# Kernel tuning notes

Measured on AMD Instinct MI355X. Metric: run time of the kernel, lower is better.

## Reference

```python
import jax, jax.numpy as jnp
import numpy as np

FRAMES, RANK = 128, 5          # rank=5 implied by create_adj6 non_adj index lists (max index 4)
N = FRAMES * RANK              # 640 nodes
B, NFEAT, NHID, NCLASS = 128, 256, 8, 16
ALPHA = 0.2                    # LeakyReLU negative slope
MASK_VAL = -9e15               # hard mask value from the torch code


def create_adj6(frames, rank):
    """Block-diagonal (with holes) + chain adjacency, exactly as in the torch source."""
    adj = np.zeros((frames * rank, frames * rank), dtype=np.float32)
    non_adj_x = [0, 0, 1, 2, 3, 3, 4, 4]
    non_adj_y = [3, 4, 4, 3, 0, 2, 0, 1]
    for i in range(frames):
        adj[rank * i:rank * (i + 1), rank * i:rank * (i + 1)] = 1
        for j in range(len(non_adj_x)):
            adj[rank * i + non_adj_x[j], rank * i + non_adj_y[j]] = 0
        for j in range(rank):
            if i > 0:
                adj[rank * i + j, rank * (i - 1) + j] = 1
            if i < frames - 1:
                adj[rank * i + j, rank * (i + 1) + j] = 1
    return adj


def _xavier(key, shape):
    fan_in, fan_out = shape[0], shape[1]
    std = np.sqrt(2.0) * np.sqrt(2.0 / (fan_in + fan_out))  # gain=sqrt(2) xavier_normal
    return std * jax.random.normal(key, shape, dtype=jnp.float32)


def setup_inputs() -> dict:
    key = jax.random.key(0)
    ks = jax.random.split(key, 7)
    x = jax.random.normal(ks[0], (B, N, NFEAT), dtype=jnp.float32)
    W1 = _xavier(ks[1], (NFEAT, NHID))
    a11 = _xavier(ks[2], (NHID, 1))
    a12 = _xavier(ks[3], (NHID, 1))
    W2 = _xavier(ks[4], (NHID, NCLASS))  # nhid*nheads=8 -> nclass=16
    a21 = _xavier(ks[5], (NCLASS, 1))
    a22 = _xavier(ks[6], (NCLASS, 1))
    adj = jnp.asarray(create_adj6(FRAMES, RANK) > 0)  # bool [N, N]
    return dict(x=x, W1=W1, a11=a11, a12=a12, W2=W2, a21=a21, a22=a22, adj=adj)


def gat_layer(xi, adj, W, a1, a2):
    # xi: [N, F_in]
    h = xi @ W                              # [N, F_out]
    f1 = h @ a1                             # [N, 1]
    f2 = h @ a2                             # [N, 1]
    e = jax.nn.leaky_relu(f1 + f2.T, negative_slope=ALPHA)  # [N, N]
    scores = jnp.where(adj, e, jnp.float32(MASK_VAL))        # hard additive-style mask
    att = jax.nn.softmax(scores, axis=-1)   # dropout disabled (eval mode)
    return att @ h                          # [N, F_out]


def reference(x, W1, a11, a12, W2, a21, a22, adj):
    def single(xi):
        h1 = gat_layer(xi, adj, W1, a11, a12)          # concat=False -> no elu inside layer
        h2 = jax.nn.elu(gat_layer(h1, adj, W2, a21, a22))
        return jax.nn.log_softmax(h2, axis=1)          # [N, NCLASS]
    return jax.vmap(single)(x)                          # [B, N, NCLASS]
```

## Files before the change

kernel.cpp:

```cpp
#include <hip/hip_runtime.h>
#include <hip/hip_bf16.h>

#define B_ 128
#define N_ 640
#define NFEAT 256
#define NHID 8
#define NCLASS 16
#define RANK 5
#define FRAMES 128
#define ALPHA 0.2f
#define PACKMASK 30236135u

#define QSPLIT 4
#define TFRAMES (FRAMES / QSPLIT)
#define TCOUNT (TFRAMES * RANK)
#define BLOCKT 384
#define MAXSTAGE 180
#define H1S 9
#define H2S 17
#define W1TS 260
#define ROWSPP (BLOCKT / 4)

__device__ __forceinline__ float lrelu(float v) { return v >= 0.0f ? v : ALPHA * v; }

__global__ void __launch_bounds__(BLOCKT, 3) k_fused(
    const float* __restrict__ x, const float* __restrict__ W1,
    const float* __restrict__ a11, const float* __restrict__ a12,
    const float* __restrict__ W2, const float* __restrict__ a21, const float* __restrict__ a22,
    float* __restrict__ out)
{
    __shared__ float smem[MAXSTAGE * H2S + 2 * MAXSTAGE + NHID * W1TS];
    float* h1s = smem;
    float* f1s = smem + MAXSTAGE * H1S;
    float* f2s = f1s + MAXSTAGE;
    float* h2s = smem;
    float* g1s = smem + MAXSTAGE * H2S;
    float* g2s = g1s + MAXSTAGE;
    float* w1t = smem + MAXSTAGE * H2S + 2 * MAXSTAGE;

    const int bid = blockIdx.x;
    const int bq  = (bid & 7) * 64 + (bid >> 3);
    const int b   = bq >> 2;
    const int q   = bq & 3;

    const int tf_lo  = q * TFRAMES;
    const int l1f_lo = max(tf_lo - 1, 0);
    const int l1f_hi = min(tf_lo + TFRAMES, FRAMES - 1);
    const int stf_lo = max(tf_lo - 2, 0);
    const int stf_hi = min(tf_lo + TFRAMES + 1, FRAMES - 1);
    const int stage_lo  = stf_lo * RANK;
    const int stage_cnt = (stf_hi - stf_lo + 1) * RANK;
    const int l1_lo  = l1f_lo * RANK;
    const int l1_cnt = (l1f_hi - l1f_lo + 1) * RANK;
    const int t_lo   = tf_lo * RANK;

    const int tid = threadIdx.x;

    for (int idx = tid; idx < NFEAT * NHID; idx += BLOCKT) {
        const int f = idx >> 3, k = idx & 7;
        w1t[k * W1TS + f] = W1[idx];
    }
    __syncthreads();

    const int sub = tid & 3;
    const int rg  = tid >> 2;
#pragma unroll
    for (int p = 0; p < 2; ++p) {
        const int row = p * ROWSPP + rg;
        if (row < stage_cnt) {
            const float* xr = x + ((size_t)b * N_ + stage_lo + row) * NFEAT;
            float4 xv[16];
#pragma unroll
            for (int t = 0; t < 16; ++t)
                xv[t] = *reinterpret_cast<const float4*>(xr + t * 16 + sub * 4);

            float h[NHID];
#pragma unroll
            for (int k = 0; k < NHID; ++k) h[k] = 0.0f;
#pragma unroll
            for (int t = 0; t < 16; ++t) {
#pragma unroll
                for (int k = 0; k < NHID; ++k) {
                    const float4 wk = *reinterpret_cast<const float4*>(
                        &w1t[k * W1TS + t * 16 + sub * 4]);
                    h[k] = fmaf(xv[t].x, wk.x, h[k]);
                    h[k] = fmaf(xv[t].y, wk.y, h[k]);
                    h[k] = fmaf(xv[t].z, wk.z, h[k]);
                    h[k] = fmaf(xv[t].w, wk.w, h[k]);
                }
            }
#pragma unroll
            for (int k = 0; k < NHID; ++k) {
                h[k] += __shfl_xor(h[k], 1, 64);
                h[k] += __shfl_xor(h[k], 2, 64);
            }
            if (sub == 0) {
                float s1 = 0.0f, s2 = 0.0f;
#pragma unroll
                for (int k = 0; k < NHID; ++k) {
                    s1 = fmaf(h[k], a11[k], s1);
                    s2 = fmaf(h[k], a12[k], s2);
                    h1s[row * H1S + k] = h[k];
                }
                f1s[row] = s1;
                f2s[row] = s2;
            }
        }
    }
    __syncthreads();

    float h2[NCLASS];
    float s1g = 0.0f, s2g = 0.0f;
    const bool actL1 = (tid < l1_cnt);
    if (actL1) {
        const int u  = l1_lo + tid;
        const int fr = u / RANK;
        const int ru = u - fr * RANK;
        const unsigned rm = (PACKMASK >> (5 * ru)) & 31u;
        const int loc      = u - stage_lo;
        const int base_loc = fr * RANK - stage_lo;
        const bool hp = (fr > 0), hn = (fr < FRAMES - 1);
        const float fu = f1s[loc];

        float m = -1e30f;
        if (hp) m = fmaxf(m, lrelu(fu + f2s[loc - RANK]));
#pragma unroll
        for (int rv = 0; rv < RANK; ++rv)
            if (rm & (1u << rv)) m = fmaxf(m, lrelu(fu + f2s[base_loc + rv]));
        if (hn) m = fmaxf(m, lrelu(fu + f2s[loc + RANK]));

        float s = 0.0f;
        float o1[NHID];
#pragma unroll
        for (int k = 0; k < NHID; ++k) o1[k] = 0.0f;

        auto acc1 = [&](int vloc) {
            float w = __expf(lrelu(fu + f2s[vloc]) - m);
            s += w;
#pragma unroll
            for (int k = 0; k < NHID; ++k) o1[k] = fmaf(w, h1s[vloc * H1S + k], o1[k]);
        };
        if (hp) acc1(loc - RANK);
#pragma unroll
        for (int rv = 0; rv < RANK; ++rv)
            if (rm & (1u << rv)) acc1(base_loc + rv);
        if (hn) acc1(loc + RANK);

        const float inv = 1.0f / s;
#pragma unroll
        for (int k = 0; k < NHID; ++k) o1[k] *= inv;

#pragma unroll
        for (int c = 0; c < NCLASS; ++c) {
            float t = 0.0f;
#pragma unroll
            for (int k = 0; k < NHID; ++k) t = fmaf(o1[k], W2[k * NCLASS + c], t);
            h2[c] = t;
            s1g = fmaf(t, a21[c], s1g);
            s2g = fmaf(t, a22[c], s2g);
        }
    }
    __syncthreads();

    if (actL1) {
        const int loc = l1_lo + tid - stage_lo;
#pragma unroll
        for (int c = 0; c < NCLASS; ++c) h2s[loc * H2S + c] = h2[c];
        g1s[loc] = s1g;
        g2s[loc] = s2g;
    }
    __syncthreads();

    if (tid < TCOUNT) {
        const int u  = t_lo + tid;
        const int fr = u / RANK;
        const int ru = u - fr * RANK;
        const unsigned rm = (PACKMASK >> (5 * ru)) & 31u;
        const int loc      = u - stage_lo;
        const int base_loc = fr * RANK - stage_lo;
        const bool hp = (fr > 0), hn = (fr < FRAMES - 1);
        const float gu = g1s[loc];

        float m = -1e30f;
        if (hp) m = fmaxf(m, lrelu(gu + g2s[loc - RANK]));
#pragma unroll
        for (int rv = 0; rv < RANK; ++rv)
            if (rm & (1u << rv)) m = fmaxf(m, lrelu(gu + g2s[base_loc + rv]));
        if (hn) m = fmaxf(m, lrelu(gu + g2s[loc + RANK]));

        float s = 0.0f;
        float o2[NCLASS];
#pragma unroll
        for (int c = 0; c < NCLASS; ++c) o2[c] = 0.0f;

        auto acc2 = [&](int vloc) {
            float w = __expf(lrelu(gu + g2s[vloc]) - m);
            s += w;
#pragma unroll
            for (int c = 0; c < NCLASS; ++c) o2[c] = fmaf(w, h2s[vloc * H2S + c], o2[c]);
        };
        if (hp) acc2(loc - RANK);
#pragma unroll
        for (int rv = 0; rv < RANK; ++rv)
            if (rm & (1u << rv)) acc2(base_loc + rv);
        if (hn) acc2(loc + RANK);

        const float inv = 1.0f / s;
#pragma unroll
        for (int c = 0; c < NCLASS; ++c) o2[c] *= inv;

#pragma unroll
        for (int c = 0; c < NCLASS; ++c) o2[c] = (o2[c] > 0.0f) ? o2[c] : __expf(o2[c]) - 1.0f;

        float mm = o2[0];
#pragma unroll
        for (int c = 1; c < NCLASS; ++c) mm = fmaxf(mm, o2[c]);
        float ss = 0.0f;
#pragma unroll
        for (int c = 0; c < NCLASS; ++c) ss += __expf(o2[c] - mm);
        const float ls = mm + __logf(ss);

        float* op = out + ((size_t)b * N_ + u) * NCLASS;
#pragma unroll
        for (int c = 0; c < NCLASS; c += 4)
            *reinterpret_cast<float4*>(op + c) =
                make_float4(o2[c] - ls, o2[c + 1] - ls, o2[c + 2] - ls, o2[c + 3] - ls);
    }
}

extern "C" void kernel_launch(void* const* d_in, const int* in_sizes, int n_in,
                              void* d_out, int out_size, void* d_ws, size_t ws_size,
                              hipStream_t stream)
{
    const float* x   = (const float*)d_in[0];
    const float* W1  = (const float*)d_in[1];
    const float* a11 = (const float*)d_in[2];
    const float* a12 = (const float*)d_in[3];
    const float* W2  = (const float*)d_in[4];
    const float* a21 = (const float*)d_in[5];
    const float* a22 = (const float*)d_in[6];
    float* outp = (float*)d_out;

    k_fused<<<B_ * QSPLIT, BLOCKT, 0, stream>>>(x, W1, a11, a12, W2, a21, a22, outp);
}
```

Before: 26.93 us.

## Split batches into eight frame chunks and compute first projection per-thread with scalar W1 loads

Doubles the sequence split to eight chunks per batch with 256-thread blocks, so there are more, smaller blocks. The first-layer projection now gives each thread one full row half of 128 features and reads W1 directly from global memory with wave-uniform (scalar) addresses. This replaces the shared-memory transposed W1 copy and the cross-lane shuffle reduction. The two halves are combined through a shared partial buffer. The smaller chunks mean more halo rows are recomputed overall, and each thread holds 16 float4 loads, which raises register pressure.

```diff
diff --git a/kernel.cpp b/kernel.cpp
--- a/kernel.cpp
+++ b/kernel.cpp
@@ -1,5 +1,4 @@
 #include <hip/hip_runtime.h>
-#include <hip/hip_bf16.h>
 
 #define B_ 128
 #define N_ 640
@@ -11,37 +10,41 @@
 #define ALPHA 0.2f
 #define PACKMASK 30236135u
 
-#define QSPLIT 4
+#define QSPLIT 8
 #define TFRAMES (FRAMES / QSPLIT)
 #define TCOUNT (TFRAMES * RANK)
-#define BLOCKT 384
-#define MAXSTAGE 180
+#define BLOCKT 256
+#define MAXSTAGE 100
 #define H1S 9
 #define H2S 17
-#define W1TS 260
-#define ROWSPP (BLOCKT / 4)
+
+#define OFF_F1S (MAXSTAGE * H1S)
+#define OFF_F2S (OFF_F1S + MAXSTAGE)
+#define OFF_HPART (OFF_F2S + MAXSTAGE)
+#define OFF_G1S (MAXSTAGE * H2S)
+#define OFF_G2S (OFF_G1S + MAXSTAGE)
+#define SMEMF (OFF_HPART + MAXSTAGE * H1S)
 
 __device__ __forceinline__ float lrelu(float v) { return v >= 0.0f ? v : ALPHA * v; }
 
-__global__ void __launch_bounds__(BLOCKT, 3) k_fused(
+__global__ void __launch_bounds__(BLOCKT, 4) k_fused(
     const float* __restrict__ x, const float* __restrict__ W1,
     const float* __restrict__ a11, const float* __restrict__ a12,
     const float* __restrict__ W2, const float* __restrict__ a21, const float* __restrict__ a22,
     float* __restrict__ out)
 {
-    __shared__ float smem[MAXSTAGE * H2S + 2 * MAXSTAGE + NHID * W1TS];
+    __shared__ float smem[SMEMF];
     float* h1s = smem;
-    float* f1s = smem + MAXSTAGE * H1S;
-    float* f2s = f1s + MAXSTAGE;
+    float* f1s = smem + OFF_F1S;
+    float* f2s = smem + OFF_F2S;
     float* h2s = smem;
-    float* g1s = smem + MAXSTAGE * H2S;
-    float* g2s = g1s + MAXSTAGE;
-    float* w1t = smem + MAXSTAGE * H2S + 2 * MAXSTAGE;
+    float* g1s = smem + OFF_G1S;
+    float* g2s = smem + OFF_G2S;
 
     const int bid = blockIdx.x;
-    const int bq  = (bid & 7) * 64 + (bid >> 3);
-    const int b   = bq >> 2;
-    const int q   = bq & 3;
+    const int bq  = (bid & 7) * 128 + (bid >> 3);
+    const int b   = bq >> 3;
+    const int q   = bq & 7;
 
     const int tf_lo  = q * TFRAMES;
     const int l1f_lo = max(tf_lo - 1, 0);
@@ -54,58 +57,65 @@
     const int l1_cnt = (l1f_hi - l1f_lo + 1) * RANK;
     const int t_lo   = tf_lo * RANK;
 
-    const int tid = threadIdx.x;
-
-    for (int idx = tid; idx < NFEAT * NHID; idx += BLOCKT) {
-        const int f = idx >> 3, k = idx & 7;
-        w1t[k * W1TS + f] = W1[idx];
-    }
-    __syncthreads();
-
-    const int sub = tid & 3;
-    const int rg  = tid >> 2;
-#pragma unroll
-    for (int p = 0; p < 2; ++p) {
-        const int row = p * ROWSPP + rg;
-        if (row < stage_cnt) {
-            const float* xr = x + ((size_t)b * N_ + stage_lo + row) * NFEAT;
-            float4 xv[16];
-#pragma unroll
-            for (int t = 0; t < 16; ++t)
-                xv[t] = *reinterpret_cast<const float4*>(xr + t * 16 + sub * 4);
-
-            float h[NHID];
-#pragma unroll
-            for (int k = 0; k < NHID; ++k) h[k] = 0.0f;
-#pragma unroll
-            for (int t = 0; t < 16; ++t) {
-#pragma unroll
-                for (int k = 0; k < NHID; ++k) {
-                    const float4 wk = *reinterpret_cast<const float4*>(
-                        &w1t[k * W1TS + t * 16 + sub * 4]);
-                    h[k] = fmaf(xv[t].x, wk.x, h[k]);
-                    h[k] = fmaf(xv[t].y, wk.y, h[k]);
-                    h[k] = fmaf(xv[t].z, wk.z, h[k]);
-                    h[k] = fmaf(xv[t].w, wk.w, h[k]);
-                }
+    const int tid  = threadIdx.x;
+    const int half = tid >> 7;
+    const int r    = tid & 127;
+
+    float h[NHID];
+#pragma unroll
+    for (int k = 0; k < NHID; ++k) h[k] = 0.0f;
+
+    if (r < stage_cnt) {
+        const float* xr = x + ((size_t)b * N_ + stage_lo + r) * NFEAT + (half << 7);
+        const float* wb = W1 + (__builtin_amdgcn_readfirstlane(half) << 10);
+
+        float4 xv[16];
+#pragma unroll
+        for (int c = 0; c < 16; ++c)
+            xv[c] = *reinterpret_cast<const float4*>(xr + 4 * c);
+#pragma unroll
+        for (int c = 0; c < 16; ++c) {
+            const float* wq = wb + (c << 5);
+#pragma unroll
+            for (int k = 0; k < NHID; ++k) {
+                h[k] = fmaf(xv[c].x, wq[k], h[k]);
+                h[k] = fmaf(xv[c].y, wq[8 + k], h[k]);
+                h[k] = fmaf(xv[c].z, wq[16 + k], h[k]);
+                h[k] = fmaf(xv[c].w, wq[24 + k], h[k]);
             }
+        }
+#pragma unroll
+        for (int c = 0; c < 16; ++c)
+            xv[c] = *reinterpret_cast<const float4*>(xr + 64 + 4 * c);
+#pragma unroll
+        for (int c = 0; c < 16; ++c) {
+            const float* wq = wb + 512 + (c << 5);
 #pragma unroll
             for (int k = 0; k < NHID; ++k) {
-                h[k] += __shfl_xor(h[k], 1, 64);
-                h[k] += __shfl_xor(h[k], 2, 64);
+                h[k] = fmaf(xv[c].x, wq[k], h[k]);
+                h[k] = fmaf(xv[c].y, wq[8 + k], h[k]);
+                h[k] = fmaf(xv[c].z, wq[16 + k], h[k]);
+                h[k] = fmaf(xv[c].w, wq[24 + k], h[k]);
             }
-            if (sub == 0) {
-                float s1 = 0.0f, s2 = 0.0f;
-#pragma unroll
-                for (int k = 0; k < NHID; ++k) {
-                    s1 = fmaf(h[k], a11[k], s1);
-                    s2 = fmaf(h[k], a12[k], s2);
-                    h1s[row * H1S + k] = h[k];
-                }
-                f1s[row] = s1;
-                f2s[row] = s2;
-            }
-        }
+        }
+        if (half) {
+#pragma unroll
+            for (int k = 0; k < NHID; ++k) smem[OFF_HPART + r * H1S + k] = h[k];
+        }
+    }
+    __syncthreads();
+
+    if (tid < stage_cnt) {
+        float s1 = 0.0f, s2 = 0.0f;
+#pragma unroll
+        for (int k = 0; k < NHID; ++k) {
+            const float v = h[k] + smem[OFF_HPART + tid * H1S + k];
+            s1 = fmaf(v, a11[k], s1);
+            s2 = fmaf(v, a12[k], s2);
+            h1s[tid * H1S + k] = v;
+        }
+        f1s[tid] = s1;
+        f2s[tid] = s2;
     }
     __syncthreads();
 
```

Result: slower. 28.32 us (+5.2%).
